# Optimization experiments

Hardware: AMD Instinct MI355X
Metric: run time of the kernel (lower is better)

Reference implementation:

```python
import jax, jax.numpy as jnp
import numpy as np

N_EMBD = 1024
HEAD_SIZE = 64
BLOCK = 4096
B = 4

def setup_inputs() -> dict:
    key = jax.random.key(0)
    k1, k2, k3, k4, k5, k6 = jax.random.split(key, 6)
    x = jax.random.normal(k1, (B, BLOCK, N_EMBD), dtype=jnp.float32)
    freqs_cos = jax.random.uniform(k2, (BLOCK, HEAD_SIZE // 2), dtype=jnp.float32)
    freqs_sin = jax.random.uniform(k3, (BLOCK, HEAD_SIZE // 2), dtype=jnp.float32)
    # bias-free Linear weights, stored as [in, out] so y = x @ W
    s = 1.0 / np.sqrt(N_EMBD)
    Wq = jax.random.normal(k4, (N_EMBD, HEAD_SIZE), dtype=jnp.float32) * s
    Wk = jax.random.normal(k5, (N_EMBD, HEAD_SIZE), dtype=jnp.float32) * s
    Wv = jax.random.normal(k6, (N_EMBD, HEAD_SIZE), dtype=jnp.float32) * s
    return {"x": x, "Wq": Wq, "Wk": Wk, "Wv": Wv,
            "freqs_cos": freqs_cos, "freqs_sin": freqs_sin}

def _rope(t, cos, sin):
    # t: [B,T,hs]; cos/sin: [T, hs//2]. Rotate consecutive (even,odd) pairs.
    tr = t[..., 0::2]
    ti = t[..., 1::2]
    cos = cos[None, :, :]
    sin = sin[None, :, :]
    out_r = tr * cos - ti * sin
    out_i = tr * sin + ti * cos
    return jnp.stack([out_r, out_i], axis=-1).reshape(t.shape)

def reference(x, Wq, Wk, Wv, freqs_cos, freqs_sin):
    B_, T, C = x.shape
    q = x @ Wq  # [B,T,hs]
    k = x @ Wk
    v = x @ Wv
    q = _rope(q, freqs_cos[:T], freqs_sin[:T])
    k = _rope(k, freqs_cos[:T], freqs_sin[:T])
    scale = k.shape[-1] ** -0.5
    wei = jnp.einsum('bqd,bkd->bqk', q, k) * scale  # [B,T,T]
    mask = jnp.tril(jnp.ones((T, T), dtype=bool))
    wei = jnp.where(mask[None], wei, -jnp.inf)
    wei = jax.nn.softmax(wei, axis=-1)
    return jnp.einsum('bqk,bkd->bqd', wei, v)
```

## Files before the change

### kernel.cpp

```cpp
#include <hip/hip_runtime.h>
#include <stdint.h>

#define TSEQ 4096
#define CEMB 1024
#define DH   64
#define NB   4
#define NCHUNK 4

typedef __attribute__((ext_vector_type(8))) short bf16x8;
typedef __attribute__((ext_vector_type(4))) float f32x4;
typedef __attribute__((ext_vector_type(4))) float f4;
typedef unsigned short u16;

__device__ __forceinline__ u16 f2bf(float f) {
  union { float f; uint32_t u; } c; c.f = f;
  uint32_t u = c.u;
  u += 0x7fffu + ((u >> 16) & 1u);
  return (u16)(u >> 16);
}

__device__ __forceinline__ int swz(int row, int colbyte) {
  return row * 128 + (colbyte ^ ((row & 7) << 4));
}

__global__ void prep_w(const float* __restrict__ Wq, const float* __restrict__ Wk,
                       const float* __restrict__ Wv, u16* __restrict__ wt) {
  int idx = blockIdx.x * 256 + threadIdx.x;
  if (idx >= 3 * DH * CEMB) return;
  int m = idx >> 16;
  int n = (idx >> 10) & 63;
  int k = idx & 1023;
  const float* W = (m == 0) ? Wq : (m == 1) ? Wk : Wv;
  wt[idx] = f2bf(W[k * DH + n]);
}

__launch_bounds__(256)
__global__ void qkv_gemm(const float* __restrict__ x, const u16* __restrict__ wt,
                         const float* __restrict__ fc, const float* __restrict__ fs,
                         u16* __restrict__ q_ws, u16* __restrict__ k_ws,
                         u16* __restrict__ vt_ws) {
  __shared__ __align__(16) u16 xs[64 * 64];
  __shared__ __align__(16) u16 wsh[192 * 64];

  const int tid  = threadIdx.x;
  const int lane = tid & 63;
  const int w    = tid >> 6;
  const int l15  = lane & 15;
  const int lhi  = lane >> 4;
  const int m0   = blockIdx.x * 64;

  const f32x4 z4 = {0.f, 0.f, 0.f, 0.f};
  f32x4 acc[12];
#pragma unroll
  for (int j = 0; j < 12; ++j) acc[j] = z4;

  for (int k0 = 0; k0 < CEMB; k0 += 64) {
    __syncthreads();
#pragma unroll
    for (int it = 0; it < 2; ++it) {
      int g = it * 256 + tid;
      int row = g >> 3, c = g & 7;
      const float* src = x + (size_t)(m0 + row) * CEMB + k0 + c * 8;
      f4 a = *(const f4*)src;
      f4 b = *(const f4*)(src + 4);
      bf16x8 v;
      v[0] = (short)f2bf(a[0]); v[1] = (short)f2bf(a[1]);
      v[2] = (short)f2bf(a[2]); v[3] = (short)f2bf(a[3]);
      v[4] = (short)f2bf(b[0]); v[5] = (short)f2bf(b[1]);
      v[6] = (short)f2bf(b[2]); v[7] = (short)f2bf(b[3]);
      *(bf16x8*)((char*)xs + swz(row, c << 4)) = v;
    }
#pragma unroll
    for (int it = 0; it < 6; ++it) {
      int g = it * 256 + tid;
      int n = g >> 3, c = g & 7;
      bf16x8 v = *(const bf16x8*)(wt + (size_t)n * CEMB + k0 + c * 8);
      *(bf16x8*)((char*)wsh + swz(n, c << 4)) = v;
    }
    __syncthreads();
#pragma unroll
    for (int kk = 0; kk < 2; ++kk) {
      bf16x8 af = *(const bf16x8*)((char*)xs + swz(w * 16 + l15, (kk * 32 + lhi * 8) * 2));
#pragma unroll
      for (int nc = 0; nc < 12; ++nc) {
        bf16x8 bfr = *(const bf16x8*)((char*)wsh + swz(nc * 16 + l15, (kk * 32 + lhi * 8) * 2));
        acc[nc] = __builtin_amdgcn_mfma_f32_16x16x32_bf16(af, bfr, acc[nc], 0, 0, 0);
      }
    }
  }

#pragma unroll
  for (int nc = 0; nc < 12; ++nc) {
    int mat = nc >> 2;
    int col = (nc & 3) * 16 + l15;
#pragma unroll
    for (int r = 0; r < 4; ++r) {
      float v = acc[nc][r];
      float o = __shfl_xor(v, 1);
      int row = m0 + w * 16 + lhi * 4 + r;
      int b = row >> 12, t = row & 4095;
      if (mat == 2) {
        vt_ws[((size_t)(b * DH + col)) * TSEQ + t] = f2bf(v);
      } else {
        int p = col >> 1;
        float cv = fc[t * 32 + p], sv = fs[t * 32 + p];
        float outv = ((col & 1) == 0) ? (v * cv - o * sv)
                                      : (o * sv + v * cv);
        u16* dst = (mat == 0) ? q_ws : k_ws;
        dst[(size_t)row * DH + col] = f2bf(outv);
      }
    }
  }
}

__launch_bounds__(256)
__global__ void attn_partial(const u16* __restrict__ q_ws, const u16* __restrict__ k_ws,
                             const u16* __restrict__ vt_ws, float* __restrict__ po,
                             float* __restrict__ pml) {
  const int qt = blockIdx.x;
  const int b  = blockIdx.y;
  const int c  = blockIdx.z;

  const int ntiles = qt + 1;
  const int cnt    = (ntiles + NCHUNK - 1) / NCHUNK;
  const int t0     = c * cnt;
  if (t0 >= ntiles) return;
  const int t1     = min(t0 + cnt, ntiles);

  __shared__ __align__(16) u16 kt[64 * 64];
  __shared__ __align__(16) u16 vts[64 * 64];
  __shared__ __align__(16) u16 pt[4][16 * 72];

  const int tid  = threadIdx.x;
  const int lane = tid & 63;
  const int w    = tid >> 6;
  const int l15  = lane & 15;
  const int lhi  = lane >> 4;
  const int q0   = qt * 64;

  const u16* qb = q_ws + (size_t)b * TSEQ * DH;
  const u16* kb = k_ws + (size_t)b * TSEQ * DH;
  const u16* vb = vt_ws + (size_t)b * DH * TSEQ;

  bf16x8 aq[2];
  {
    int qrow = q0 + w * 16 + l15;
#pragma unroll
    for (int kk = 0; kk < 2; ++kk)
      aq[kk] = *(const bf16x8*)(qb + (size_t)qrow * DH + kk * 32 + lhi * 8);
  }

  const f32x4 z4 = {0.f, 0.f, 0.f, 0.f};
  f32x4 oacc[4] = {z4, z4, z4, z4};
  float m_r[4], l_r[4];
#pragma unroll
  for (int r = 0; r < 4; ++r) { m_r[r] = -1e30f; l_r[r] = 0.f; }

  const int myqbase = q0 + w * 16 + lhi * 4;

  for (int kv = t0; kv < t1; ++kv) {
    const int kv0 = kv * 64;
    __syncthreads();
#pragma unroll
    for (int it = 0; it < 2; ++it) {
      int g = it * 256 + tid;
      int row = g >> 3, cc = g & 7;
      bf16x8 vk = *(const bf16x8*)(kb + (size_t)(kv0 + row) * DH + cc * 8);
      *(bf16x8*)((char*)kt + swz(row, cc << 4)) = vk;
      bf16x8 vv = *(const bf16x8*)(vb + (size_t)row * TSEQ + kv0 + cc * 8);
      *(bf16x8*)((char*)vts + swz(row, cc << 4)) = vv;
    }
    __syncthreads();

    f32x4 sacc[4] = {z4, z4, z4, z4};
#pragma unroll
    for (int kk = 0; kk < 2; ++kk) {
#pragma unroll
      for (int cb = 0; cb < 4; ++cb) {
        bf16x8 bk = *(const bf16x8*)((char*)kt + swz(cb * 16 + l15, (kk * 32 + lhi * 8) * 2));
        sacc[cb] = __builtin_amdgcn_mfma_f32_16x16x32_bf16(aq[kk], bk, sacc[cb], 0, 0, 0);
      }
    }
#pragma unroll
    for (int cb = 0; cb < 4; ++cb)
#pragma unroll
      for (int r = 0; r < 4; ++r) {
        int ki = kv0 + cb * 16 + l15;
        int qi = myqbase + r;
        float sv = sacc[cb][r] * 0.125f;
        sacc[cb][r] = (ki <= qi) ? sv : -1e30f;
      }
    float mx[4];
#pragma unroll
    for (int r = 0; r < 4; ++r)
      mx[r] = fmaxf(fmaxf(sacc[0][r], sacc[1][r]), fmaxf(sacc[2][r], sacc[3][r]));
#pragma unroll
    for (int s = 1; s <= 8; s <<= 1)
#pragma unroll
      for (int r = 0; r < 4; ++r) mx[r] = fmaxf(mx[r], __shfl_xor(mx[r], s));
    float fac[4];
#pragma unroll
    for (int r = 0; r < 4; ++r) {
      float mn = fmaxf(m_r[r], mx[r]);
      fac[r] = __expf(m_r[r] - mn);
      m_r[r] = mn;
    }
    float rs[4] = {0.f, 0.f, 0.f, 0.f};
#pragma unroll
    for (int cb = 0; cb < 4; ++cb)
#pragma unroll
      for (int r = 0; r < 4; ++r) {
        float p = __expf(sacc[cb][r] - m_r[r]);
        sacc[cb][r] = p;
        rs[r] += p;
      }
#pragma unroll
    for (int s = 1; s <= 8; s <<= 1)
#pragma unroll
      for (int r = 0; r < 4; ++r) rs[r] += __shfl_xor(rs[r], s);
#pragma unroll
    for (int r = 0; r < 4; ++r) l_r[r] = l_r[r] * fac[r] + rs[r];
#pragma unroll
    for (int nc = 0; nc < 4; ++nc)
#pragma unroll
      for (int r = 0; r < 4; ++r) oacc[nc][r] *= fac[r];
#pragma unroll
    for (int cb = 0; cb < 4; ++cb)
#pragma unroll
      for (int r = 0; r < 4; ++r)
        pt[w][(lhi * 4 + r) * 72 + cb * 16 + l15] = f2bf(sacc[cb][r]);
    bf16x8 ap[2];
#pragma unroll
    for (int kk = 0; kk < 2; ++kk)
      ap[kk] = *(const bf16x8*)(&pt[w][l15 * 72 + kk * 32 + lhi * 8]);
#pragma unroll
    for (int kk = 0; kk < 2; ++kk)
#pragma unroll
      for (int nc = 0; nc < 4; ++nc) {
        bf16x8 bv = *(const bf16x8*)((char*)vts + swz(nc * 16 + l15, (kk * 32 + lhi * 8) * 2));
        oacc[nc] = __builtin_amdgcn_mfma_f32_16x16x32_bf16(ap[kk], bv, oacc[nc], 0, 0, 0);
      }
  }

  const int slot = ((b * 64 + qt) * NCHUNK + c);
  float* o_out = po + (size_t)slot * (64 * 64);
#pragma unroll
  for (int nc = 0; nc < 4; ++nc)
#pragma unroll
    for (int r = 0; r < 4; ++r) {
      int rloc = w * 16 + lhi * 4 + r;
      o_out[rloc * 64 + nc * 16 + l15] = oacc[nc][r];
    }
#pragma unroll
  for (int r = 0; r < 4; ++r) {
    if (l15 == 0) {
      int rloc = w * 16 + lhi * 4 + r;
      pml[(size_t)slot * 128 + rloc]      = m_r[r];
      pml[(size_t)slot * 128 + 64 + rloc] = l_r[r];
    }
  }
}

__launch_bounds__(256)
__global__ void attn_combine(const float* __restrict__ po, const float* __restrict__ pml,
                             float* __restrict__ out) {
  int idx = blockIdx.x * 256 + threadIdx.x;
  int d   = idx & 63;
  int t   = (idx >> 6) & 4095;
  int b   = idx >> 18;
  int qt  = t >> 6;
  int rloc = t & 63;
  int ntiles = qt + 1;
  int cnt = (ntiles + NCHUNK - 1) / NCHUNK;

  float m_c[NCHUNK], l_c[NCHUNK], o_c[NCHUNK];
  float M = -1e30f;
#pragma unroll
  for (int c = 0; c < NCHUNK; ++c) {
    bool valid = (c * cnt < ntiles);
    int slot = ((b * 64 + qt) * NCHUNK + c);
    m_c[c] = valid ? pml[(size_t)slot * 128 + rloc]      : -1e30f;
    l_c[c] = valid ? pml[(size_t)slot * 128 + 64 + rloc] : 0.f;
    o_c[c] = valid ? po[(size_t)slot * (64 * 64) + rloc * 64 + d] : 0.f;
    M = fmaxf(M, m_c[c]);
  }
  float den = 0.f, num = 0.f;
#pragma unroll
  for (int c = 0; c < NCHUNK; ++c) {
    float e = __expf(m_c[c] - M);
    den += e * l_c[c];
    num += e * o_c[c];
  }
  out[idx] = num / den;
}

extern "C" void kernel_launch(void* const* d_in, const int* in_sizes, int n_in,
                              void* d_out, int out_size, void* d_ws, size_t ws_size,
                              hipStream_t stream) {
  const float* x  = (const float*)d_in[0];
  const float* Wq = (const float*)d_in[1];
  const float* Wk = (const float*)d_in[2];
  const float* Wv = (const float*)d_in[3];
  const float* fc = (const float*)d_in[4];
  const float* fs = (const float*)d_in[5];
  float* out = (float*)d_out;

  char* ws = (char*)d_ws;
  u16*   wt    = (u16*)(ws);
  u16*   q_ws  = (u16*)(ws + (1u << 19));
  u16*   k_ws  = (u16*)(ws + (1u << 19) + (1u << 21));
  u16*   vt_ws = (u16*)(ws + (1u << 19) + (2u << 21));
  float* po    = (float*)(ws + (1u << 19) + (3u << 21));
  float* pml   = (float*)(ws + (1u << 19) + (3u << 21) + (1u << 24));

  prep_w<<<(3 * DH * CEMB + 255) / 256, 256, 0, stream>>>(Wq, Wk, Wv, wt);
  qkv_gemm<<<dim3(256), 256, 0, stream>>>(x, wt, fc, fs, q_ws, k_ws, vt_ws);
  attn_partial<<<dim3(64, NB, NCHUNK), 256, 0, stream>>>(q_ws, k_ws, vt_ws, po, pml);
  attn_combine<<<dim3((NB * TSEQ * DH) / 256), 256, 0, stream>>>(po, pml, out);
}
```

Baseline: 187.5 us.

## Double-buffer QKV GEMM and attention tiles, halve GEMM M-tile, coalesce weight prep

```diff
diff --git a/kernel.cpp b/kernel.cpp
--- a/kernel.cpp
+++ b/kernel.cpp
@@ -28,76 +28,91 @@
   int idx = blockIdx.x * 256 + threadIdx.x;
   if (idx >= 3 * DH * CEMB) return;
   int m = idx >> 16;
-  int n = (idx >> 10) & 63;
-  int k = idx & 1023;
+  int r = idx & 65535;
+  int k = r >> 6, n = r & 63;
   const float* W = (m == 0) ? Wq : (m == 1) ? Wk : Wv;
-  wt[idx] = f2bf(W[k * DH + n]);
-}
+  wt[(size_t)m * 65536 + n * 1024 + k] = f2bf(W[r]);
+}
+
+#define QKV_LOADX(K0) { \
+    const float* s_ = x + (size_t)(m0 + xrow) * CEMB + (K0) + xc * 8; \
+    xa = *(const f4*)s_; xb = *(const f4*)(s_ + 4); }
+#define QKV_LOADW(K0) \
+    _Pragma("unroll") for (int it = 0; it < 6; ++it) { \
+      int gg = it * 256 + tid; \
+      wv[it] = *(const bf16x8*)(wt + (size_t)(gg >> 3) * CEMB + (K0) + (gg & 7) * 8); }
+#define QKV_STORE(BUF) { \
+    bf16x8 xv_; \
+    xv_[0] = (short)f2bf(xa[0]); xv_[1] = (short)f2bf(xa[1]); \
+    xv_[2] = (short)f2bf(xa[2]); xv_[3] = (short)f2bf(xa[3]); \
+    xv_[4] = (short)f2bf(xb[0]); xv_[5] = (short)f2bf(xb[1]); \
+    xv_[6] = (short)f2bf(xb[2]); xv_[7] = (short)f2bf(xb[3]); \
+    *(bf16x8*)((char*)xs[BUF] + swz(xrow, xc << 4)) = xv_; \
+    _Pragma("unroll") for (int it = 0; it < 6; ++it) { \
+      int gg = it * 256 + tid; \
+      *(bf16x8*)((char*)wsh[BUF] + swz(gg >> 3, (gg & 7) << 4)) = wv[it]; } }
 
 __launch_bounds__(256)
 __global__ void qkv_gemm(const float* __restrict__ x, const u16* __restrict__ wt,
                          const float* __restrict__ fc, const float* __restrict__ fs,
                          u16* __restrict__ q_ws, u16* __restrict__ k_ws,
                          u16* __restrict__ vt_ws) {
-  __shared__ __align__(16) u16 xs[64 * 64];
-  __shared__ __align__(16) u16 wsh[192 * 64];
+  __shared__ __align__(16) u16 xs[2][32 * 64];
+  __shared__ __align__(16) u16 wsh[2][192 * 64];
 
   const int tid  = threadIdx.x;
   const int lane = tid & 63;
   const int w    = tid >> 6;
   const int l15  = lane & 15;
   const int lhi  = lane >> 4;
-  const int m0   = blockIdx.x * 64;
+  const int rg   = w & 1;
+  const int cg   = w >> 1;
+  const int m0   = blockIdx.x * 32;
+  const int xrow = tid >> 3, xc = tid & 7;
 
   const f32x4 z4 = {0.f, 0.f, 0.f, 0.f};
-  f32x4 acc[12];
-#pragma unroll
-  for (int j = 0; j < 12; ++j) acc[j] = z4;
-
-  for (int k0 = 0; k0 < CEMB; k0 += 64) {
+  f32x4 acc[6];
+#pragma unroll
+  for (int j = 0; j < 6; ++j) acc[j] = z4;
+
+  f4 xa, xb;
+  bf16x8 wv[6];
+
+  QKV_LOADX(0)
+  QKV_LOADW(0)
+  QKV_STORE(0)
+  __syncthreads();
+
+  for (int ks = 0; ks < CEMB / 64; ++ks) {
+    const int cur  = ks & 1;
+    const bool more = (ks + 1 < CEMB / 64);
+    if (more) {
+      QKV_LOADX((ks + 1) * 64)
+      QKV_LOADW((ks + 1) * 64)
+    }
+#pragma unroll
+    for (int kk = 0; kk < 2; ++kk) {
+      bf16x8 af = *(const bf16x8*)((char*)xs[cur] + swz(rg * 16 + l15, (kk * 32 + lhi * 8) * 2));
+#pragma unroll
+      for (int nc = 0; nc < 6; ++nc) {
+        bf16x8 bfr = *(const bf16x8*)((char*)wsh[cur] + swz(cg * 96 + nc * 16 + l15, (kk * 32 + lhi * 8) * 2));
+        acc[nc] = __builtin_amdgcn_mfma_f32_16x16x32_bf16(af, bfr, acc[nc], 0, 0, 0);
+      }
+    }
+    if (more) QKV_STORE(cur ^ 1)
     __syncthreads();
-#pragma unroll
-    for (int it = 0; it < 2; ++it) {
-      int g = it * 256 + tid;
-      int row = g >> 3, c = g & 7;
-      const float* src = x + (size_t)(m0 + row) * CEMB + k0 + c * 8;
-      f4 a = *(const f4*)src;
-      f4 b = *(const f4*)(src + 4);
-      bf16x8 v;
-      v[0] = (short)f2bf(a[0]); v[1] = (short)f2bf(a[1]);
-      v[2] = (short)f2bf(a[2]); v[3] = (short)f2bf(a[3]);
-      v[4] = (short)f2bf(b[0]); v[5] = (short)f2bf(b[1]);
-      v[6] = (short)f2bf(b[2]); v[7] = (short)f2bf(b[3]);
-      *(bf16x8*)((char*)xs + swz(row, c << 4)) = v;
-    }
-#pragma unroll
-    for (int it = 0; it < 6; ++it) {
-      int g = it * 256 + tid;
-      int n = g >> 3, c = g & 7;
-      bf16x8 v = *(const bf16x8*)(wt + (size_t)n * CEMB + k0 + c * 8);
-      *(bf16x8*)((char*)wsh + swz(n, c << 4)) = v;
-    }
-    __syncthreads();
-#pragma unroll
-    for (int kk = 0; kk < 2; ++kk) {
-      bf16x8 af = *(const bf16x8*)((char*)xs + swz(w * 16 + l15, (kk * 32 + lhi * 8) * 2));
-#pragma unroll
-      for (int nc = 0; nc < 12; ++nc) {
-        bf16x8 bfr = *(const bf16x8*)((char*)wsh + swz(nc * 16 + l15, (kk * 32 + lhi * 8) * 2));
-        acc[nc] = __builtin_amdgcn_mfma_f32_16x16x32_bf16(af, bfr, acc[nc], 0, 0, 0);
-      }
-    }
-  }
-
-#pragma unroll
-  for (int nc = 0; nc < 12; ++nc) {
-    int mat = nc >> 2;
-    int col = (nc & 3) * 16 + l15;
+  }
+
+#pragma unroll
+  for (int nc = 0; nc < 6; ++nc) {
+    int gcol = cg * 96 + nc * 16 + l15;
+    int mat  = gcol >> 6;
+    int col  = gcol & 63;
 #pragma unroll
     for (int r = 0; r < 4; ++r) {
       float v = acc[nc][r];
       float o = __shfl_xor(v, 1);
-      int row = m0 + w * 16 + lhi * 4 + r;
+      int row = m0 + rg * 16 + lhi * 4 + r;
       int b = row >> 12, t = row & 4095;
       if (mat == 2) {
         vt_ws[((size_t)(b * DH + col)) * TSEQ + t] = f2bf(v);
@@ -113,6 +128,17 @@
   }
 }
 
+#define ATT_LOADKV(KV0) \
+    _Pragma("unroll") for (int it = 0; it < 2; ++it) { \
+      int gg = it * 256 + tid, row_ = gg >> 3, cc_ = gg & 7; \
+      kreg[it] = *(const bf16x8*)(kb + (size_t)((KV0) + row_) * DH + cc_ * 8); \
+      vreg[it] = *(const bf16x8*)(vb + (size_t)row_ * TSEQ + (KV0) + cc_ * 8); }
+#define ATT_WRITEKV(BUF) \
+    _Pragma("unroll") for (int it = 0; it < 2; ++it) { \
+      int gg = it * 256 + tid, row_ = gg >> 3, cc_ = gg & 7; \
+      *(bf16x8*)((char*)kt[BUF] + swz(row_, cc_ << 4)) = kreg[it]; \
+      *(bf16x8*)((char*)vts[BUF] + swz(row_, cc_ << 4)) = vreg[it]; }
+
 __launch_bounds__(256)
 __global__ void attn_partial(const u16* __restrict__ q_ws, const u16* __restrict__ k_ws,
                              const u16* __restrict__ vt_ws, float* __restrict__ po,
@@ -126,10 +152,11 @@
   const int t0     = c * cnt;
   if (t0 >= ntiles) return;
   const int t1     = min(t0 + cnt, ntiles);
-
-  __shared__ __align__(16) u16 kt[64 * 64];
-  __shared__ __align__(16) u16 vts[64 * 64];
-  __shared__ __align__(16) u16 pt[4][16 * 72];
+  const int nst    = t1 - t0;
+
+  __shared__ __align__(16) u16 kt[2][64 * 64];
+  __shared__ __align__(16) u16 vts[2][64 * 64];
+  __shared__ __align__(16) u16 pt2[4 * 16 * 64];
 
   const int tid  = threadIdx.x;
   const int lane = tid & 63;
@@ -141,6 +168,7 @@
   const u16* qb = q_ws + (size_t)b * TSEQ * DH;
   const u16* kb = k_ws + (size_t)b * TSEQ * DH;
   const u16* vb = vt_ws + (size_t)b * DH * TSEQ;
+  char* ptw = (char*)pt2 + w * 2048;
 
   bf16x8 aq[2];
   {
@@ -158,26 +186,24 @@
 
   const int myqbase = q0 + w * 16 + lhi * 4;
 
-  for (int kv = t0; kv < t1; ++kv) {
-    const int kv0 = kv * 64;
-    __syncthreads();
-#pragma unroll
-    for (int it = 0; it < 2; ++it) {
-      int g = it * 256 + tid;
-      int row = g >> 3, cc = g & 7;
-      bf16x8 vk = *(const bf16x8*)(kb + (size_t)(kv0 + row) * DH + cc * 8);
-      *(bf16x8*)((char*)kt + swz(row, cc << 4)) = vk;
-      bf16x8 vv = *(const bf16x8*)(vb + (size_t)row * TSEQ + kv0 + cc * 8);
-      *(bf16x8*)((char*)vts + swz(row, cc << 4)) = vv;
-    }
-    __syncthreads();
+  bf16x8 kreg[2], vreg[2];
+
+  ATT_LOADKV(t0 * 64)
+  ATT_WRITEKV(0)
+  __syncthreads();
+
+  for (int i = 0; i < nst; ++i) {
+    const int kv0 = (t0 + i) * 64;
+    const int cur = i & 1;
+    const bool more = (i + 1 < nst);
+    if (more) ATT_LOADKV((t0 + i + 1) * 64)
 
     f32x4 sacc[4] = {z4, z4, z4, z4};
 #pragma unroll
     for (int kk = 0; kk < 2; ++kk) {
 #pragma unroll
       for (int cb = 0; cb < 4; ++cb) {
-        bf16x8 bk = *(const bf16x8*)((char*)kt + swz(cb * 16 + l15, (kk * 32 + lhi * 8) * 2));
+        bf16x8 bk = *(const bf16x8*)((char*)kt[cur] + swz(cb * 16 + l15, (kk * 32 + lhi * 8) * 2));
         sacc[cb] = __builtin_amdgcn_mfma_f32_16x16x32_bf16(aq[kk], bk, sacc[cb], 0, 0, 0);
       }
     }
@@ -228,18 +254,21 @@
     for (int cb = 0; cb < 4; ++cb)
 #pragma unroll
       for (int r = 0; r < 4; ++r)
-        pt[w][(lhi * 4 + r) * 72 + cb * 16 + l15] = f2bf(sacc[cb][r]);
+        *(u16*)(ptw + swz(lhi * 4 + r, (cb * 16 + l15) * 2)) = f2bf(sacc[cb][r]);
     bf16x8 ap[2];
 #pragma unroll
     for (int kk = 0; kk < 2; ++kk)
-      ap[kk] = *(const bf16x8*)(&pt[w][l15 * 72 + kk * 32 + lhi * 8]);
+      ap[kk] = *(const bf16x8*)(ptw + swz(l15, (kk * 32 + lhi * 8) * 2));
 #pragma unroll
     for (int kk = 0; kk < 2; ++kk)
 #pragma unroll
       for (int nc = 0; nc < 4; ++nc) {
-        bf16x8 bv = *(const bf16x8*)((char*)vts + swz(nc * 16 + l15, (kk * 32 + lhi * 8) * 2));
+        bf16x8 bv = *(const bf16x8*)((char*)vts[cur] + swz(nc * 16 + l15, (kk * 32 + lhi * 8) * 2));
         oacc[nc] = __builtin_amdgcn_mfma_f32_16x16x32_bf16(ap[kk], bv, oacc[nc], 0, 0, 0);
       }
+
+    if (more) ATT_WRITEKV(cur ^ 1)
+    __syncthreads();
   }
 
   const int slot = ((b * 64 + qt) * NCHUNK + c);
@@ -314,7 +343,7 @@
   float* pml   = (float*)(ws + (1u << 19) + (3u << 21) + (1u << 24));
 
   prep_w<<<(3 * DH * CEMB + 255) / 256, 256, 0, stream>>>(Wq, Wk, Wv, wt);
-  qkv_gemm<<<dim3(256), 256, 0, stream>>>(x, wt, fc, fs, q_ws, k_ws, vt_ws);
+  qkv_gemm<<<dim3(512), 256, 0, stream>>>(x, wt, fc, fs, q_ws, k_ws, vt_ws);
   attn_partial<<<dim3(64, NB, NCHUNK), 256, 0, stream>>>(q_ws, k_ws, vt_ws, po, pml);
   attn_combine<<<dim3((NB * TSEQ * DH) / 256), 256, 0, stream>>>(po, pml, out);
 }
```

New measurement: 180.4 us. 3.8% less time.
